# Kernel tuning notes

Measured on AMD Instinct MI355X. Metric: run time of the kernel, lower is better.

## Reference

```python
import jax, jax.numpy as jnp
import numpy as np

H = 5          # hidden units per LSTMCell (hardcoded in source)
F = 64         # input feature dim
T = 100        # seq_len (hardcoded in source)
B = 16384      # batch
OUT = 3        # dense output units


def setup_inputs() -> dict:
    key = jax.random.key(0)
    ks = jax.random.split(key, 12)
    s = 0.1
    return {
        "x":  jax.random.normal(ks[0], (B, T, F), dtype=jnp.float32),
        # layer 1: input F -> hidden H, keras kernel layout [in, 4H] gate order i,f,c,o
        "W1": jax.random.normal(ks[1], (F, 4 * H), dtype=jnp.float32) * s,
        "U1": jax.random.normal(ks[2], (H, 4 * H), dtype=jnp.float32) * s,
        "b1": jax.random.normal(ks[3], (4 * H,), dtype=jnp.float32) * s,
        # layer 2: H -> H
        "W2": jax.random.normal(ks[4], (H, 4 * H), dtype=jnp.float32) * s,
        "U2": jax.random.normal(ks[5], (H, 4 * H), dtype=jnp.float32) * s,
        "b2": jax.random.normal(ks[6], (4 * H,), dtype=jnp.float32) * s,
        # layer 3: H -> H
        "W3": jax.random.normal(ks[7], (H, 4 * H), dtype=jnp.float32) * s,
        "U3": jax.random.normal(ks[8], (H, 4 * H), dtype=jnp.float32) * s,
        "b3": jax.random.normal(ks[9], (4 * H,), dtype=jnp.float32) * s,
        # final dense: H -> OUT
        "Wd": jax.random.normal(ks[10], (H, OUT), dtype=jnp.float32) * s,
        "bd": jax.random.normal(ks[11], (OUT,), dtype=jnp.float32) * s,
    }


def _lstm_layer(seq, W, U, b):
    """Run one keras-style LSTMCell over time. seq: [B,T,Din] -> [B,T,H]."""
    # precompute input contribution for all timesteps: [B,T,4H]
    xz = jnp.einsum("btd,dk->btk", seq, W) + b
    xz_t = jnp.swapaxes(xz, 0, 1)  # [T,B,4H]
    b_sz = seq.shape[0]
    h0 = jnp.zeros((b_sz, H), dtype=seq.dtype)
    c0 = jnp.zeros((b_sz, H), dtype=seq.dtype)

    def step(carry, zx):
        h, c = carry
        z = zx + h @ U  # [B,4H]
        i = jax.nn.sigmoid(z[:, 0 * H:1 * H])
        f = jax.nn.sigmoid(z[:, 1 * H:2 * H])
        g = jnp.tanh(z[:, 2 * H:3 * H])
        o = jax.nn.sigmoid(z[:, 3 * H:4 * H])
        c_new = f * c + i * g
        h_new = o * jnp.tanh(c_new)
        return (h_new, c_new), h_new

    (_, _), hs = jax.lax.scan(step, (h0, c0), xz_t)
    return jnp.swapaxes(hs, 0, 1)  # [B,T,H]


def reference(x, W1, U1, b1, W2, U2, b2, W3, U3, b3, Wd, bd):
    s1 = _lstm_layer(x, W1, U1, b1)    # [B,T,H]
    s2 = _lstm_layer(s1, W2, U2, b2)   # [B,T,H]
    s3 = _lstm_layer(s2, W3, U3, b3)   # [B,T,H]
    last = s3[:, -1, :]                # only final hidden of layer 3 is used
    return last @ Wd + bd              # [B,OUT]
```

## Files before the change

### kernel.cpp

```cpp
#include <hip/hip_runtime.h>
#include <cstddef>

#define BB   16384
#define TT_  100
#define FF   64
#define K4   20
#define NOUT 3

__device__ __forceinline__ float sigf(float x) {
    return __builtin_amdgcn_rcpf(1.0f + __expf(-x));
}
__device__ __forceinline__ float tanhf_fast(float x) {
    return 1.0f - 2.0f * __builtin_amdgcn_rcpf(__expf(2.0f * x) + 1.0f);
}
template <int IMM>
__device__ __forceinline__ float swz(float v) {
    return __int_as_float(__builtin_amdgcn_ds_swizzle(__float_as_int(v), IMM));
}

template <int NT>
__device__ __forceinline__ void rec_steps(
    float (&zbuf)[8][K4][9], int g, int ue,
    const float (&u1w)[4][5], const float (&w2w)[4][5], const float (&u2w)[4][5],
    const float (&w3w)[4][5], const float (&u3w)[4][5],
    const float (&bb1)[4], const float (&bb2)[4], const float (&bb3)[4],
    float (&h1)[5], float (&h2)[5], float (&h3)[5],
    float &c1, float &c2, float &c3)
{
#pragma unroll
    for (int s = 0; s < NT; ++s) {
        float z[4];
#pragma unroll
        for (int j = 0; j < 4; ++j) {
            float acc = zbuf[s][j * 5 + ue][g] + bb1[j];
#pragma unroll
            for (int d = 0; d < 5; ++d) acc = fmaf(h1[d], u1w[j][d], acc);
            z[j] = acc;
        }
        {
            const float iv = sigf(z[0]), fv = sigf(z[1]);
            const float gv = tanhf_fast(z[2]), ov = sigf(z[3]);
            c1 = fmaf(fv, c1, iv * gv);
            const float ho = ov * tanhf_fast(c1);
            h1[0] = swz<0x018>(ho); h1[1] = swz<0x038>(ho);
            h1[2] = swz<0x058>(ho); h1[3] = swz<0x078>(ho);
            h1[4] = swz<0x098>(ho);
        }
#pragma unroll
        for (int j = 0; j < 4; ++j) {
            float acc = bb2[j];
#pragma unroll
            for (int d = 0; d < 5; ++d) acc = fmaf(h1[d], w2w[j][d], acc);
#pragma unroll
            for (int d = 0; d < 5; ++d) acc = fmaf(h2[d], u2w[j][d], acc);
            z[j] = acc;
        }
        {
            const float iv = sigf(z[0]), fv = sigf(z[1]);
            const float gv = tanhf_fast(z[2]), ov = sigf(z[3]);
            c2 = fmaf(fv, c2, iv * gv);
            const float ho = ov * tanhf_fast(c2);
            h2[0] = swz<0x018>(ho); h2[1] = swz<0x038>(ho);
            h2[2] = swz<0x058>(ho); h2[3] = swz<0x078>(ho);
            h2[4] = swz<0x098>(ho);
        }
#pragma unroll
        for (int j = 0; j < 4; ++j) {
            float acc = bb3[j];
#pragma unroll
            for (int d = 0; d < 5; ++d) acc = fmaf(h2[d], w3w[j][d], acc);
#pragma unroll
            for (int d = 0; d < 5; ++d) acc = fmaf(h3[d], u3w[j][d], acc);
            z[j] = acc;
        }
        {
            const float iv = sigf(z[0]), fv = sigf(z[1]);
            const float gv = tanhf_fast(z[2]), ov = sigf(z[3]);
            c3 = fmaf(fv, c3, iv * gv);
            const float ho = ov * tanhf_fast(c3);
            h3[0] = swz<0x018>(ho); h3[1] = swz<0x038>(ho);
            h3[2] = swz<0x058>(ho); h3[3] = swz<0x078>(ho);
            h3[4] = swz<0x098>(ho);
        }
    }
}

__global__ __launch_bounds__(64) __attribute__((amdgpu_waves_per_eu(2, 2)))
void fused_lstm_kernel(
    const float* __restrict__ x,
    const float* __restrict__ W1, const float* __restrict__ U1, const float* __restrict__ b1,
    const float* __restrict__ W2, const float* __restrict__ U2, const float* __restrict__ b2,
    const float* __restrict__ W3, const float* __restrict__ U3, const float* __restrict__ b3,
    const float* __restrict__ Wd, const float* __restrict__ bd,
    float* __restrict__ out)
{
    __shared__ float sWT[K4][FF];
    __shared__ float zbuf[8][K4][9];

    const int lane = threadIdx.x;
    const int g    = lane >> 3;
    const int u    = lane & 7;
    const int ue   = (u < 5) ? u : 4;
    const int tq   = (lane >> 1) & 3;
    const int fh   = lane & 1;
    const int b    = blockIdx.x * 8 + g;

    const float* xp0 = x + ((size_t)b * TT_ + tq) * FF + fh * 32;
    const float* xp1 = xp0 + 4 * FF;
    float4 xa0[8], xa1[8];
#pragma unroll
    for (int fc = 0; fc < 8; ++fc) xa0[fc] = ((const float4*)xp0)[fc];
#pragma unroll
    for (int fc = 0; fc < 8; ++fc) xa1[fc] = ((const float4*)xp1)[fc];

#pragma unroll
    for (int w = 0; w < 20; ++w) {
        int i = w * 64 + lane;
        sWT[i % K4][i / K4] = W1[i];
    }

    float u1w[4][5], w2w[4][5], u2w[4][5], w3w[4][5], u3w[4][5];
    float bb1[4], bb2[4], bb3[4];
#pragma unroll
    for (int j = 0; j < 4; ++j) {
        const int k = j * 5 + ue;
#pragma unroll
        for (int d = 0; d < 5; ++d) {
            u1w[j][d] = U1[d * K4 + k];
            w2w[j][d] = W2[d * K4 + k];
            u2w[j][d] = U2[d * K4 + k];
            w3w[j][d] = W3[d * K4 + k];
            u3w[j][d] = U3[d * K4 + k];
        }
        bb1[j] = b1[k];
        bb2[j] = b2[k];
        bb3[j] = b3[k];
    }
    const int uo = (u < NOUT) ? u : 0;
    float wdw[5];
    const float bdw = bd[uo];
#pragma unroll
    for (int d = 0; d < 5; ++d) wdw[d] = Wd[d * NOUT + uo];

    float h1[5] = {0,0,0,0,0}, h2[5] = {0,0,0,0,0}, h3[5] = {0,0,0,0,0};
    float c1 = 0.f, c2 = 0.f, c3 = 0.f;

    const int t1 = tq + (fh << 2);

    for (int c = 0; c < 13; ++c) {
#pragma unroll 4
        for (int k = 0; k < K4; ++k) {
            float a0 = 0.f, a1 = 0.f;
#pragma unroll
            for (int fc = 0; fc < 8; ++fc) {
                const float4 wv = *(const float4*)&sWT[k][fh * 32 + fc * 4];
                const float4 x0 = xa0[fc];
                const float4 x1 = xa1[fc];
                a0 = fmaf(x0.x, wv.x, fmaf(x0.y, wv.y, fmaf(x0.z, wv.z, fmaf(x0.w, wv.w, a0))));
                a1 = fmaf(x1.x, wv.x, fmaf(x1.y, wv.y, fmaf(x1.z, wv.z, fmaf(x1.w, wv.w, a1))));
            }
            a0 += swz<0x041F>(a0);
            a1 += swz<0x041F>(a1);
            zbuf[t1][k][g] = fh ? a1 : a0;
        }

        if (c < 12) {
            xp0 += 8 * FF;
            xp1 = (c == 11) ? xp0 : (xp1 + 8 * FF);
#pragma unroll
            for (int fc = 0; fc < 8; ++fc) xa0[fc] = ((const float4*)xp0)[fc];
#pragma unroll
            for (int fc = 0; fc < 8; ++fc) xa1[fc] = ((const float4*)xp1)[fc];
        }

        if (c < 12) {
            rec_steps<8>(zbuf, g, ue, u1w, w2w, u2w, w3w, u3w,
                         bb1, bb2, bb3, h1, h2, h3, c1, c2, c3);
        } else {
            rec_steps<4>(zbuf, g, ue, u1w, w2w, u2w, w3w, u3w,
                         bb1, bb2, bb3, h1, h2, h3, c1, c2, c3);
        }
    }

    if (u < NOUT) {
        float s = bdw;
#pragma unroll
        for (int d = 0; d < 5; ++d) s = fmaf(h3[d], wdw[d], s);
        out[b * NOUT + u] = s;
    }
}

extern "C" void kernel_launch(void* const* d_in, const int* in_sizes, int n_in,
                              void* d_out, int out_size, void* d_ws, size_t ws_size,
                              hipStream_t stream) {
    const float* x   = (const float*)d_in[0];
    const float* W1  = (const float*)d_in[1];
    const float* U1  = (const float*)d_in[2];
    const float* b1  = (const float*)d_in[3];
    const float* W2  = (const float*)d_in[4];
    const float* U2  = (const float*)d_in[5];
    const float* b2  = (const float*)d_in[6];
    const float* W3  = (const float*)d_in[7];
    const float* U3  = (const float*)d_in[8];
    const float* b3  = (const float*)d_in[9];
    const float* Wd  = (const float*)d_in[10];
    const float* bdp = (const float*)d_in[11];
    float* out = (float*)d_out;

    fused_lstm_kernel<<<BB / 8, 64, 0, stream>>>(
        x, W1, U1, b1, W2, U2, b2, W3, U3, b3, Wd, bdp, out);
}
```

Measured before the change: 628.9 us.

## Split fused LSTM into projection kernel and one-batch-per-lane recurrence kernel

Splits the single fused kernel in two. The first kernel computes the input projection x·W1+b1 for every timestep and writes it to workspace in [T,B,20] layout. The second kernel runs the three-layer recurrence with one batch element per lane, keeping all gates in registers and dropping the cross-lane swizzles and the idle lanes of the old 8-lanes-per-sample mapping. The cost is an extra global round trip of about 131 MB of intermediate z, plus heavy register use and only 256 single-wave blocks in the recurrence kernel, which may limit latency hiding.

```diff
diff --git a/kernel.cpp b/kernel.cpp
--- a/kernel.cpp
+++ b/kernel.cpp
@@ -5,6 +5,7 @@
 #define TT_  100
 #define FF   64
 #define K4   20
+#define HH   5
 #define NOUT 3
 
 __device__ __forceinline__ float sigf(float x) {
@@ -13,180 +14,190 @@
 __device__ __forceinline__ float tanhf_fast(float x) {
     return 1.0f - 2.0f * __builtin_amdgcn_rcpf(__expf(2.0f * x) + 1.0f);
 }
-template <int IMM>
-__device__ __forceinline__ float swz(float v) {
-    return __int_as_float(__builtin_amdgcn_ds_swizzle(__float_as_int(v), IMM));
-}
-
-template <int NT>
-__device__ __forceinline__ void rec_steps(
-    float (&zbuf)[8][K4][9], int g, int ue,
-    const float (&u1w)[4][5], const float (&w2w)[4][5], const float (&u2w)[4][5],
-    const float (&w3w)[4][5], const float (&u3w)[4][5],
-    const float (&bb1)[4], const float (&bb2)[4], const float (&bb3)[4],
-    float (&h1)[5], float (&h2)[5], float (&h3)[5],
-    float &c1, float &c2, float &c3)
+
+__global__ __launch_bounds__(64, 2) void proj_kernel(
+    const float* __restrict__ x, const float* __restrict__ W1,
+    const float* __restrict__ b1, float* __restrict__ z)
 {
-#pragma unroll
-    for (int s = 0; s < NT; ++s) {
-        float z[4];
-#pragma unroll
-        for (int j = 0; j < 4; ++j) {
-            float acc = zbuf[s][j * 5 + ue][g] + bb1[j];
-#pragma unroll
-            for (int d = 0; d < 5; ++d) acc = fmaf(h1[d], u1w[j][d], acc);
-            z[j] = acc;
-        }
-        {
-            const float iv = sigf(z[0]), fv = sigf(z[1]);
-            const float gv = tanhf_fast(z[2]), ov = sigf(z[3]);
-            c1 = fmaf(fv, c1, iv * gv);
-            const float ho = ov * tanhf_fast(c1);
-            h1[0] = swz<0x018>(ho); h1[1] = swz<0x038>(ho);
-            h1[2] = swz<0x058>(ho); h1[3] = swz<0x078>(ho);
-            h1[4] = swz<0x098>(ho);
-        }
-#pragma unroll
-        for (int j = 0; j < 4; ++j) {
-            float acc = bb2[j];
-#pragma unroll
-            for (int d = 0; d < 5; ++d) acc = fmaf(h1[d], w2w[j][d], acc);
-#pragma unroll
-            for (int d = 0; d < 5; ++d) acc = fmaf(h2[d], u2w[j][d], acc);
-            z[j] = acc;
-        }
-        {
-            const float iv = sigf(z[0]), fv = sigf(z[1]);
-            const float gv = tanhf_fast(z[2]), ov = sigf(z[3]);
-            c2 = fmaf(fv, c2, iv * gv);
-            const float ho = ov * tanhf_fast(c2);
-            h2[0] = swz<0x018>(ho); h2[1] = swz<0x038>(ho);
-            h2[2] = swz<0x058>(ho); h2[3] = swz<0x078>(ho);
-            h2[4] = swz<0x098>(ho);
-        }
-#pragma unroll
-        for (int j = 0; j < 4; ++j) {
-            float acc = bb3[j];
-#pragma unroll
-            for (int d = 0; d < 5; ++d) acc = fmaf(h2[d], w3w[j][d], acc);
-#pragma unroll
-            for (int d = 0; d < 5; ++d) acc = fmaf(h3[d], u3w[j][d], acc);
-            z[j] = acc;
-        }
-        {
-            const float iv = sigf(z[0]), fv = sigf(z[1]);
-            const float gv = tanhf_fast(z[2]), ov = sigf(z[3]);
-            c3 = fmaf(fv, c3, iv * gv);
-            const float ho = ov * tanhf_fast(c3);
-            h3[0] = swz<0x018>(ho); h3[1] = swz<0x038>(ho);
-            h3[2] = swz<0x058>(ho); h3[3] = swz<0x078>(ho);
-            h3[4] = swz<0x098>(ho);
-        }
-    }
-}
-
-__global__ __launch_bounds__(64) __attribute__((amdgpu_waves_per_eu(2, 2)))
-void fused_lstm_kernel(
-    const float* __restrict__ x,
-    const float* __restrict__ W1, const float* __restrict__ U1, const float* __restrict__ b1,
+    __shared__ float sWT[K4][FF];
+    const int lane = threadIdx.x;
+    const int tloc = lane >> 3;
+    const int g    = lane & 7;
+    const int b    = blockIdx.x * 8 + g;
+
+#pragma unroll
+    for (int w = 0; w < 20; ++w) {
+        int i = w * 64 + lane;
+        sWT[i % K4][i / K4] = W1[i];
+    }
+    float bz[K4];
+#pragma unroll
+    for (int k = 0; k < K4; ++k) bz[k] = b1[k];
+    __syncthreads();
+
+    const float4* xrow = (const float4*)(x + ((size_t)b * TT_ + tloc) * FF);
+    float4 xa[16], xb[16];
+#pragma unroll
+    for (int i = 0; i < 16; ++i) xa[i] = xrow[i];
+
+    for (int c = 0; c < 13; ++c) {
+        if (c < 12) {
+            int tn = c * 8 + 8 + tloc; if (tn > TT_ - 1) tn = TT_ - 1;
+            const float4* p = (const float4*)(x + ((size_t)b * TT_ + tn) * FF);
+#pragma unroll
+            for (int i = 0; i < 16; ++i) xb[i] = p[i];
+        }
+        const int t = c * 8 + tloc;
+        float zr[K4];
+#pragma unroll
+        for (int k = 0; k < K4; ++k) {
+            float a0 = bz[k], a1 = 0.f, a2 = 0.f, a3 = 0.f;
+#pragma unroll
+            for (int p = 0; p < 4; ++p) {
+                const float4 w0 = *(const float4*)&sWT[k][p * 16 + 0];
+                const float4 w1 = *(const float4*)&sWT[k][p * 16 + 4];
+                const float4 w2 = *(const float4*)&sWT[k][p * 16 + 8];
+                const float4 w3 = *(const float4*)&sWT[k][p * 16 + 12];
+                const float4 x0 = xa[p * 4 + 0], x1 = xa[p * 4 + 1];
+                const float4 x2 = xa[p * 4 + 2], x3 = xa[p * 4 + 3];
+                a0 = fmaf(x0.w, w0.w, fmaf(x0.z, w0.z, fmaf(x0.y, w0.y, fmaf(x0.x, w0.x, a0))));
+                a1 = fmaf(x1.w, w1.w, fmaf(x1.z, w1.z, fmaf(x1.y, w1.y, fmaf(x1.x, w1.x, a1))));
+                a2 = fmaf(x2.w, w2.w, fmaf(x2.z, w2.z, fmaf(x2.y, w2.y, fmaf(x2.x, w2.x, a2))));
+                a3 = fmaf(x3.w, w3.w, fmaf(x3.z, w3.z, fmaf(x3.y, w3.y, fmaf(x3.x, w3.x, a3))));
+            }
+            zr[k] = (a0 + a1) + (a2 + a3);
+        }
+        if (t < TT_) {
+            float4* zp = (float4*)(z + ((size_t)t * BB + b) * K4);
+#pragma unroll
+            for (int q = 0; q < 5; ++q)
+                zp[q] = make_float4(zr[4 * q], zr[4 * q + 1], zr[4 * q + 2], zr[4 * q + 3]);
+        }
+#pragma unroll
+        for (int i = 0; i < 16; ++i) xa[i] = xb[i];
+    }
+}
+
+__global__ __launch_bounds__(64) __attribute__((amdgpu_waves_per_eu(1, 1)))
+void rec_kernel(
+    const float* __restrict__ z,
+    const float* __restrict__ U1,
     const float* __restrict__ W2, const float* __restrict__ U2, const float* __restrict__ b2,
     const float* __restrict__ W3, const float* __restrict__ U3, const float* __restrict__ b3,
     const float* __restrict__ Wd, const float* __restrict__ bd,
     float* __restrict__ out)
 {
-    __shared__ float sWT[K4][FF];
-    __shared__ float zbuf[8][K4][9];
-
+    __shared__ float sW3T[K4][8];
+    __shared__ float sU3T[K4][8];
     const int lane = threadIdx.x;
-    const int g    = lane >> 3;
-    const int u    = lane & 7;
-    const int ue   = (u < 5) ? u : 4;
-    const int tq   = (lane >> 1) & 3;
-    const int fh   = lane & 1;
-    const int b    = blockIdx.x * 8 + g;
-
-    const float* xp0 = x + ((size_t)b * TT_ + tq) * FF + fh * 32;
-    const float* xp1 = xp0 + 4 * FF;
-    float4 xa0[8], xa1[8];
-#pragma unroll
-    for (int fc = 0; fc < 8; ++fc) xa0[fc] = ((const float4*)xp0)[fc];
-#pragma unroll
-    for (int fc = 0; fc < 8; ++fc) xa1[fc] = ((const float4*)xp1)[fc];
-
-#pragma unroll
-    for (int w = 0; w < 20; ++w) {
-        int i = w * 64 + lane;
-        sWT[i % K4][i / K4] = W1[i];
-    }
-
-    float u1w[4][5], w2w[4][5], u2w[4][5], w3w[4][5], u3w[4][5];
-    float bb1[4], bb2[4], bb3[4];
-#pragma unroll
-    for (int j = 0; j < 4; ++j) {
-        const int k = j * 5 + ue;
-#pragma unroll
-        for (int d = 0; d < 5; ++d) {
-            u1w[j][d] = U1[d * K4 + k];
-            w2w[j][d] = W2[d * K4 + k];
-            u2w[j][d] = U2[d * K4 + k];
-            w3w[j][d] = W3[d * K4 + k];
-            u3w[j][d] = U3[d * K4 + k];
-        }
-        bb1[j] = b1[k];
-        bb2[j] = b2[k];
-        bb3[j] = b3[k];
-    }
-    const int uo = (u < NOUT) ? u : 0;
-    float wdw[5];
-    const float bdw = bd[uo];
-#pragma unroll
-    for (int d = 0; d < 5; ++d) wdw[d] = Wd[d * NOUT + uo];
-
-    float h1[5] = {0,0,0,0,0}, h2[5] = {0,0,0,0,0}, h3[5] = {0,0,0,0,0};
-    float c1 = 0.f, c2 = 0.f, c3 = 0.f;
-
-    const int t1 = tq + (fh << 2);
-
-    for (int c = 0; c < 13; ++c) {
-#pragma unroll 4
-        for (int k = 0; k < K4; ++k) {
-            float a0 = 0.f, a1 = 0.f;
-#pragma unroll
-            for (int fc = 0; fc < 8; ++fc) {
-                const float4 wv = *(const float4*)&sWT[k][fh * 32 + fc * 4];
-                const float4 x0 = xa0[fc];
-                const float4 x1 = xa1[fc];
-                a0 = fmaf(x0.x, wv.x, fmaf(x0.y, wv.y, fmaf(x0.z, wv.z, fmaf(x0.w, wv.w, a0))));
-                a1 = fmaf(x1.x, wv.x, fmaf(x1.y, wv.y, fmaf(x1.z, wv.z, fmaf(x1.w, wv.w, a1))));
-            }
-            a0 += swz<0x041F>(a0);
-            a1 += swz<0x041F>(a1);
-            zbuf[t1][k][g] = fh ? a1 : a0;
-        }
-
-        if (c < 12) {
-            xp0 += 8 * FF;
-            xp1 = (c == 11) ? xp0 : (xp1 + 8 * FF);
-#pragma unroll
-            for (int fc = 0; fc < 8; ++fc) xa0[fc] = ((const float4*)xp0)[fc];
-#pragma unroll
-            for (int fc = 0; fc < 8; ++fc) xa1[fc] = ((const float4*)xp1)[fc];
-        }
-
-        if (c < 12) {
-            rec_steps<8>(zbuf, g, ue, u1w, w2w, u2w, w3w, u3w,
-                         bb1, bb2, bb3, h1, h2, h3, c1, c2, c3);
-        } else {
-            rec_steps<4>(zbuf, g, ue, u1w, w2w, u2w, w3w, u3w,
-                         bb1, bb2, bb3, h1, h2, h3, c1, c2, c3);
-        }
-    }
-
-    if (u < NOUT) {
-        float s = bdw;
-#pragma unroll
-        for (int d = 0; d < 5; ++d) s = fmaf(h3[d], wdw[d], s);
-        out[b * NOUT + u] = s;
+    const size_t b = (size_t)blockIdx.x * 64 + lane;
+
+    for (int i = lane; i < 100; i += 64) {
+        sW3T[i % K4][i / K4] = W3[i];
+        sU3T[i % K4][i / K4] = U3[i];
+    }
+    if (lane < K4) { sW3T[lane][5] = b2[lane]; sU3T[lane][5] = b3[lane]; }
+    __syncthreads();
+
+    float u1r[HH][K4], w2r[HH][K4], u2r[HH][K4];
+#pragma unroll
+    for (int d = 0; d < HH; ++d)
+#pragma unroll
+        for (int k = 0; k < K4; ++k) {
+            u1r[d][k] = U1[d * K4 + k];
+            w2r[d][k] = W2[d * K4 + k];
+            u2r[d][k] = U2[d * K4 + k];
+        }
+
+    float h1[HH] = {}, h2[HH] = {}, h3[HH] = {};
+    float c1[HH] = {}, c2[HH] = {}, c3[HH] = {};
+
+    float4 zc[5];
+    {
+        const float4* zp = (const float4*)(z + b * K4);
+#pragma unroll
+        for (int q = 0; q < 5; ++q) zc[q] = zp[q];
+    }
+
+#pragma unroll 2
+    for (int t = 0; t < TT_; ++t) {
+        float4 zn[5];
+        if (t < TT_ - 1) {
+            const float4* zp = (const float4*)(z + ((size_t)(t + 1) * BB + b) * K4);
+#pragma unroll
+            for (int q = 0; q < 5; ++q) zn[q] = zp[q];
+        }
+        float zt[K4];
+#pragma unroll
+        for (int q = 0; q < 5; ++q) {
+            zt[4 * q + 0] = zc[q].x; zt[4 * q + 1] = zc[q].y;
+            zt[4 * q + 2] = zc[q].z; zt[4 * q + 3] = zc[q].w;
+        }
+
+        float zl[K4];
+#pragma unroll
+        for (int k = 0; k < K4; ++k) {
+            float a = zt[k];
+#pragma unroll
+            for (int d = 0; d < HH; ++d) a = fmaf(h1[d], u1r[d][k], a);
+            zl[k] = a;
+        }
+#pragma unroll
+        for (int u = 0; u < HH; ++u) {
+            const float iv = sigf(zl[u]),        fv = sigf(zl[5 + u]);
+            const float gv = tanhf_fast(zl[10 + u]), ov = sigf(zl[15 + u]);
+            c1[u] = fmaf(fv, c1[u], iv * gv);
+            h1[u] = ov * tanhf_fast(c1[u]);
+        }
+#pragma unroll
+        for (int k = 0; k < K4; ++k) {
+            float a = sW3T[k][5];
+#pragma unroll
+            for (int d = 0; d < HH; ++d) a = fmaf(h1[d], w2r[d][k], a);
+#pragma unroll
+            for (int d = 0; d < HH; ++d) a = fmaf(h2[d], u2r[d][k], a);
+            zl[k] = a;
+        }
+#pragma unroll
+        for (int u = 0; u < HH; ++u) {
+            const float iv = sigf(zl[u]),        fv = sigf(zl[5 + u]);
+            const float gv = tanhf_fast(zl[10 + u]), ov = sigf(zl[15 + u]);
+            c2[u] = fmaf(fv, c2[u], iv * gv);
+            h2[u] = ov * tanhf_fast(c2[u]);
+        }
+#pragma unroll
+        for (int k = 0; k < K4; ++k) {
+            const float4 w3q = *(const float4*)&sW3T[k][0];
+            const float4 u3q = *(const float4*)&sU3T[k][0];
+            float a = sU3T[k][5];
+            a = fmaf(h2[0], w3q.x, a); a = fmaf(h2[1], w3q.y, a);
+            a = fmaf(h2[2], w3q.z, a); a = fmaf(h2[3], w3q.w, a);
+            a = fmaf(h2[4], sW3T[k][4], a);
+            a = fmaf(h3[0], u3q.x, a); a = fmaf(h3[1], u3q.y, a);
+            a = fmaf(h3[2], u3q.z, a); a = fmaf(h3[3], u3q.w, a);
+            a = fmaf(h3[4], sU3T[k][4], a);
+            zl[k] = a;
+        }
+#pragma unroll
+        for (int u = 0; u < HH; ++u) {
+            const float iv = sigf(zl[u]),        fv = sigf(zl[5 + u]);
+            const float gv = tanhf_fast(zl[10 + u]), ov = sigf(zl[15 + u]);
+            c3[u] = fmaf(fv, c3[u], iv * gv);
+            h3[u] = ov * tanhf_fast(c3[u]);
+        }
+
+        if (t < TT_ - 1) {
+#pragma unroll
+            for (int q = 0; q < 5; ++q) zc[q] = zn[q];
+        }
+    }
+
+#pragma unroll
+    for (int o = 0; o < NOUT; ++o) {
+        float s = bd[o];
+#pragma unroll
+        for (int d = 0; d < HH; ++d) s = fmaf(h3[d], Wd[d * NOUT + o], s);
+        out[b * NOUT + o] = s;
     }
 }
 
@@ -207,6 +218,8 @@
     const float* bdp = (const float*)d_in[11];
     float* out = (float*)d_out;
 
-    fused_lstm_kernel<<<BB / 8, 64, 0, stream>>>(
-        x, W1, U1, b1, W2, U2, b2, W3, U3, b3, Wd, bdp, out);
-}
+    float* zws = (float*)d_ws;
+
+    proj_kernel<<<BB / 8, 64, 0, stream>>>(x, W1, b1, zws);
+    rec_kernel<<<BB / 64, 64, 0, stream>>>(zws, U1, W2, U2, b2, W3, U3, b3, Wd, bdp, out);
+}
```

Result: slower. 2.234 ms (+255.2%).
